# Kernel optimization log

Hardware: AMD Instinct MI355X
Metric: run time of the kernel (lower is better)

The kernel has to match this reference:

```python
import jax, jax.numpy as jnp
import numpy as np


def _pad_amounts(n, bs):
    p = (bs - n % bs) % bs
    return p // 2, p - p // 2  # (front, back); matches torch logic for even/odd


def _reset_forward(x, leftm, rightm):
    bs = leftm.shape[0]
    H, W = x.shape[-2], x.shape[-1]
    a, b = _pad_amounts(H, bs)
    c, d = _pad_amounts(W, bs)
    if a or b or c or d:
        pad = [(0, 0)] * (x.ndim - 2) + [(a, b), (c, d)]
        x = jnp.pad(x, pad)
    identity = x
    Hp, Wp = x.shape[-2], x.shape[-1]
    Hc, Wc = Hp // bs, Wp // bs
    # chunk along last dim -> contiguous slices == reshape (Wp -> bs, Wc)
    xb = x.reshape(x.shape[:-1] + (bs, Wc))          # [..., Hp, bs, Wc]
    y = jnp.einsum('ji,...iw->...jw', leftm, xb)     # out chunk j = sum_i L[j,i]*chunk_i
    y = y.reshape(x.shape[:-1] + (Wp,))              # [..., Hp, Wp]
    # chunk along dim -2 -> reshape (Hp -> bs, Hc)
    yb = y.reshape(y.shape[:-2] + (bs, Hc, Wp))      # [..., bs, Hc, Wp]
    z = jnp.einsum('ij,...ihw->...jhw', rightm, yb)  # out chunk j = sum_i R[i,j]*chunk_i (rightm^T rows)
    z = z.reshape(y.shape)                           # [..., Hp, Wp]
    return z + identity


def setup_inputs() -> dict:
    key = jax.random.key(0)
    kx, kl, kr = jax.random.split(key, 3)
    bs = 10
    x = jax.random.normal(kx, (16, 2000, 2000), dtype=jnp.float32)
    leftm = jax.random.normal(kl, (bs, bs), dtype=jnp.float32)
    rightm = jax.random.normal(kr, (bs, bs), dtype=jnp.float32)
    return {"x": x, "leftm": leftm, "rightm": rightm}


def reference(x, leftm, rightm):
    return _reset_forward(x, leftm, rightm)
```

## Files before the change

kernel.cpp:

```cpp
#include <hip/hip_runtime.h>


#define IMG   2000
#define BSZ   10
#define TC    200
#define CHW   (IMG * IMG)
#define NW4   (TC / 4)
#define RPITCH 12

__global__ __launch_bounds__(512, 4)
void reset_rowline(const float* __restrict__ x,
                   const float* __restrict__ leftm,
                   const float* __restrict__ rightm,
                   float* __restrict__ out)
{
    __shared__ __align__(16) float4 Ysh[BSZ * BSZ * NW4];
    __shared__ __align__(16) float  Rts[BSZ * RPITCH];

    const int t = threadIdx.x;
    if (t < BSZ * RPITCH) {
        const int jh = t / RPITCH, c = t - jh * RPITCH;
        Rts[t] = (c < BSZ) ? rightm[c * BSZ + jh] : 0.0f;
    }

    const int bid = blockIdx.x;
    const int b   = bid / TC;
    const int h   = bid % TC;

    const int  ih     = t / NW4;
    const int  wo4    = t - ih * NW4;
    const bool active = (t < BSZ * NW4);

    float4 x4[BSZ];
    const float4* rowp = nullptr;
    if (active) {
        rowp = (const float4*)(x + (size_t)b * CHW + (size_t)(ih * TC + h) * IMG);
        #pragma unroll
        for (int iw = 0; iw < BSZ; ++iw)
            x4[iw] = rowp[iw * NW4 + wo4];
    }

    if (active) {
        #pragma unroll
        for (int jw = 0; jw < BSZ; ++jw) {
            const float l0 = leftm[jw * BSZ + 0];
            float4 y;
            y.x = l0 * x4[0].x; y.y = l0 * x4[0].y;
            y.z = l0 * x4[0].z; y.w = l0 * x4[0].w;
            #pragma unroll
            for (int iw = 1; iw < BSZ; ++iw) {
                const float l = leftm[jw * BSZ + iw];
                y.x += l * x4[iw].x; y.y += l * x4[iw].y;
                y.z += l * x4[iw].z; y.w += l * x4[iw].w;
            }
            Ysh[(ih * BSZ + jw) * NW4 + wo4] = y;
        }
    }

    __syncthreads();

    if (active) {
        const int jh = ih;
        float r[BSZ];
        {
            const float4 ra = *(const float4*)&Rts[jh * RPITCH + 0];
            const float4 rb = *(const float4*)&Rts[jh * RPITCH + 4];
            const float4 rc = *(const float4*)&Rts[jh * RPITCH + 8];
            r[0] = ra.x; r[1] = ra.y; r[2] = ra.z; r[3] = ra.w;
            r[4] = rb.x; r[5] = rb.y; r[6] = rb.z; r[7] = rb.w;
            r[8] = rc.x; r[9] = rc.y;
        }
        #pragma unroll
        for (int ihp = 0; ihp < BSZ; ++ihp) {
            const float rr = r[ihp];
            #pragma unroll
            for (int jw = 0; jw < BSZ; ++jw) {
                const float4 y = Ysh[(ihp * BSZ + jw) * NW4 + wo4];
                x4[jw].x += rr * y.x; x4[jw].y += rr * y.y;
                x4[jw].z += rr * y.z; x4[jw].w += rr * y.w;
            }
        }
        float4* orow = (float4*)(out + (size_t)b * CHW + (size_t)(jh * TC + h) * IMG);
        #pragma unroll
        for (int jw = 0; jw < BSZ; ++jw)
            orow[jw * NW4 + wo4] = x4[jw];
    }
}

extern "C" void kernel_launch(void* const* d_in, const int* in_sizes, int n_in,
                              void* d_out, int out_size, void* d_ws, size_t ws_size,
                              hipStream_t stream) {
    const float* x = (const float*)d_in[0];
    const float* L = (const float*)d_in[1];
    const float* R = (const float*)d_in[2];
    float* out = (float*)d_out;
    reset_rowline<<<3200, 512, 0, stream>>>(x, L, R, out);
}
```

Baseline: 421.2 us.

## Convert to persistent grid with register double-buffered row prefetch

Launches a fixed grid of 512 blocks that loop over all 3200 row-lines, prefetching the next line's input into a second register buffer while computing the current one. The rightm column is loaded straight into registers instead of staged through shared memory, and a lighter custom barrier replaces __syncthreads. The aim is to hide global load latency behind compute and cut block launch overhead. The trade-off is doubled register use for the input tiles and fewer resident blocks per CU, which could lower memory-level parallelism.

```diff
diff --git a/kernel.cpp b/kernel.cpp
--- a/kernel.cpp
+++ b/kernel.cpp
@@ -1,89 +1,106 @@
 #include <hip/hip_runtime.h>
 
 
-#define IMG   2000
-#define BSZ   10
-#define TC    200
-#define CHW   (IMG * IMG)
-#define NW4   (TC / 4)
-#define RPITCH 12
+#define IMG    2000
+#define BSZ    10
+#define TC     200
+#define CHW    (IMG * IMG)
+#define NW4    (TC / 4)
+#define NLINES (16 * TC)
+#define GRID   512
+
+#define BAR() do { asm volatile("s_waitcnt lgkmcnt(0)" ::: "memory"); \
+                   __builtin_amdgcn_s_barrier();                      \
+                   asm volatile("" ::: "memory"); } while (0)
 
 __global__ __launch_bounds__(512, 4)
-void reset_rowline(const float* __restrict__ x,
-                   const float* __restrict__ leftm,
-                   const float* __restrict__ rightm,
-                   float* __restrict__ out)
+void reset_pipe(const float* __restrict__ x,
+                const float* __restrict__ leftm,
+                const float* __restrict__ rightm,
+                float* __restrict__ out)
 {
     __shared__ __align__(16) float4 Ysh[BSZ * BSZ * NW4];
-    __shared__ __align__(16) float  Rts[BSZ * RPITCH];
 
-    const int t = threadIdx.x;
-    if (t < BSZ * RPITCH) {
-        const int jh = t / RPITCH, c = t - jh * RPITCH;
-        Rts[t] = (c < BSZ) ? rightm[c * BSZ + jh] : 0.0f;
-    }
-
-    const int bid = blockIdx.x;
-    const int b   = bid / TC;
-    const int h   = bid % TC;
-
+    const int  t      = threadIdx.x;
     const int  ih     = t / NW4;
     const int  wo4    = t - ih * NW4;
     const bool active = (t < BSZ * NW4);
+    const int  jh     = active ? ih : 0;
 
-    float4 x4[BSZ];
-    const float4* rowp = nullptr;
+    float r[BSZ];
+    #pragma unroll
+    for (int ihp = 0; ihp < BSZ; ++ihp)
+        r[ihp] = rightm[ihp * BSZ + jh];
+
+    float4 xc[BSZ], xn[BSZ];
+    int g = blockIdx.x;
+
     if (active) {
-        rowp = (const float4*)(x + (size_t)b * CHW + (size_t)(ih * TC + h) * IMG);
+        const int b = g / TC, h = g - b * TC;
+        const float4* rowp =
+            (const float4*)(x + (size_t)b * CHW + (size_t)(ih * TC + h) * IMG);
         #pragma unroll
         for (int iw = 0; iw < BSZ; ++iw)
-            x4[iw] = rowp[iw * NW4 + wo4];
+            xc[iw] = rowp[iw * NW4 + wo4];
     }
 
-    if (active) {
-        #pragma unroll
-        for (int jw = 0; jw < BSZ; ++jw) {
-            const float l0 = leftm[jw * BSZ + 0];
-            float4 y;
-            y.x = l0 * x4[0].x; y.y = l0 * x4[0].y;
-            y.z = l0 * x4[0].z; y.w = l0 * x4[0].w;
+    while (true) {
+        const int gn = g + GRID;
+
+        if (gn < NLINES && active) {
+            const int bn = gn / TC, hn = gn - bn * TC;
+            const float4* rowp =
+                (const float4*)(x + (size_t)bn * CHW + (size_t)(ih * TC + hn) * IMG);
             #pragma unroll
-            for (int iw = 1; iw < BSZ; ++iw) {
-                const float l = leftm[jw * BSZ + iw];
-                y.x += l * x4[iw].x; y.y += l * x4[iw].y;
-                y.z += l * x4[iw].z; y.w += l * x4[iw].w;
-            }
-            Ysh[(ih * BSZ + jw) * NW4 + wo4] = y;
+            for (int iw = 0; iw < BSZ; ++iw)
+                xn[iw] = rowp[iw * NW4 + wo4];
         }
-    }
 
-    __syncthreads();
-
-    if (active) {
-        const int jh = ih;
-        float r[BSZ];
-        {
-            const float4 ra = *(const float4*)&Rts[jh * RPITCH + 0];
-            const float4 rb = *(const float4*)&Rts[jh * RPITCH + 4];
-            const float4 rc = *(const float4*)&Rts[jh * RPITCH + 8];
-            r[0] = ra.x; r[1] = ra.y; r[2] = ra.z; r[3] = ra.w;
-            r[4] = rb.x; r[5] = rb.y; r[6] = rb.z; r[7] = rb.w;
-            r[8] = rc.x; r[9] = rc.y;
-        }
-        #pragma unroll
-        for (int ihp = 0; ihp < BSZ; ++ihp) {
-            const float rr = r[ihp];
+        if (active) {
             #pragma unroll
             for (int jw = 0; jw < BSZ; ++jw) {
-                const float4 y = Ysh[(ihp * BSZ + jw) * NW4 + wo4];
-                x4[jw].x += rr * y.x; x4[jw].y += rr * y.y;
-                x4[jw].z += rr * y.z; x4[jw].w += rr * y.w;
+                const float l0 = leftm[jw * BSZ + 0];
+                float4 y;
+                y.x = l0 * xc[0].x; y.y = l0 * xc[0].y;
+                y.z = l0 * xc[0].z; y.w = l0 * xc[0].w;
+                #pragma unroll
+                for (int iw = 1; iw < BSZ; ++iw) {
+                    const float l = leftm[jw * BSZ + iw];
+                    y.x += l * xc[iw].x; y.y += l * xc[iw].y;
+                    y.z += l * xc[iw].z; y.w += l * xc[iw].w;
+                }
+                Ysh[(ih * BSZ + jw) * NW4 + wo4] = y;
             }
         }
-        float4* orow = (float4*)(out + (size_t)b * CHW + (size_t)(jh * TC + h) * IMG);
+
+        BAR();
+
+        if (active) {
+            #pragma unroll
+            for (int ihp = 0; ihp < BSZ; ++ihp) {
+                const float rr = r[ihp];
+                #pragma unroll
+                for (int jw = 0; jw < BSZ; ++jw) {
+                    const float4 y = Ysh[(ihp * BSZ + jw) * NW4 + wo4];
+                    xc[jw].x += rr * y.x; xc[jw].y += rr * y.y;
+                    xc[jw].z += rr * y.z; xc[jw].w += rr * y.w;
+                }
+            }
+            const int b = g / TC, h = g - b * TC;
+            float4* orow =
+                (float4*)(out + (size_t)b * CHW + (size_t)(jh * TC + h) * IMG);
+            #pragma unroll
+            for (int jw = 0; jw < BSZ; ++jw)
+                orow[jw * NW4 + wo4] = xc[jw];
+        }
+
+        if (gn >= NLINES) break;
+
+        BAR();
+
         #pragma unroll
-        for (int jw = 0; jw < BSZ; ++jw)
-            orow[jw * NW4 + wo4] = x4[jw];
+        for (int i = 0; i < BSZ; ++i) xc[i] = xn[i];
+        g = gn;
     }
 }
 
@@ -94,5 +111,5 @@
     const float* L = (const float*)d_in[1];
     const float* R = (const float*)d_in[2];
     float* out = (float*)d_out;
-    reset_rowline<<<3200, 512, 0, stream>>>(x, L, R, out);
+    reset_pipe<<<GRID, 512, 0, stream>>>(x, L, R, out);
 }
```

Result: slower. 459.5 us (+9.1%).
